# Kernel optimization log

Measured on AMD Instinct MI355X. Metric: run time of the kernel, lower is better.

The kernel has to match this reference:

```python
import math
import jax, jax.numpy as jnp
import numpy as np

B, S, D, H = 2, 2048, 2048, 16
HD = D // H  # head_dim = 128


def setup_inputs() -> dict:
    key = jax.random.key(0)
    ks = jax.random.split(key, 5)
    x = jax.random.normal(ks[0], (B, S, D), dtype=jnp.float32)
    # torch nn.Linear weights are [out_features, in_features]
    wq = jax.random.normal(ks[1], (D, D), dtype=jnp.float32) * 0.02
    wk = jax.random.normal(ks[2], (D, D), dtype=jnp.float32) * 0.02
    wv = jax.random.normal(ks[3], (D, D), dtype=jnp.float32) * 0.02
    wo = jax.random.normal(ks[4], (D, D), dtype=jnp.float32) * 0.02
    # llama-style rotary frequencies: freq_cis[t, i] = exp(1j * t / 10000^(2i/hd))
    inv_freq = 1.0 / (10000.0 ** (jnp.arange(0, HD, 2, dtype=jnp.float32) / HD))  # [HD/2]
    angles = jnp.arange(S, dtype=jnp.float32)[:, None] * inv_freq[None, :]  # [S, HD/2]
    freq_cos = jnp.cos(angles)
    freq_sin = jnp.sin(angles)
    # additive causal mask (0 on/below diagonal, large negative above)
    mask = jnp.triu(jnp.full((S, S), -1e9, dtype=jnp.float32), k=1)
    return {"x": x, "wq": wq, "wk": wk, "wv": wv, "wo": wo,
            "freq_cos": freq_cos, "freq_sin": freq_sin, "mask": mask}


def _rope(t, cos, sin):
    # t: [B, H, S, HD]; cos/sin: [S, HD/2]. Consecutive pairs form complex numbers.
    b, h, s, hd = t.shape
    tr = t.reshape(b, h, s, hd // 2, 2)
    re, im = tr[..., 0], tr[..., 1]
    c = cos[None, None, :, :]
    sn = sin[None, None, :, :]
    out_re = re * c - im * sn
    out_im = re * sn + im * c
    return jnp.stack([out_re, out_im], axis=-1).reshape(b, h, s, hd)


def reference(x, wq, wk, wv, wo, freq_cos, freq_sin, mask):
    b, s, d = x.shape
    hd = 2 * freq_cos.shape[-1]
    h = wq.shape[0] // hd
    # projections (torch Linear: y = x @ W.T)
    q = jnp.einsum('bsd,ed->bse', x, wq).reshape(b, s, h, hd).transpose(0, 2, 1, 3)
    k = jnp.einsum('bsd,ed->bse', x, wk).reshape(b, s, h, hd).transpose(0, 2, 1, 3)
    v = jnp.einsum('bsd,ed->bse', x, wv).reshape(b, s, h, hd).transpose(0, 2, 1, 3)
    q = _rope(q, freq_cos, freq_sin)
    k = _rope(k, freq_cos, freq_sin)
    scores = jnp.einsum('bhqd,bhkd->bhqk', q, k) / math.sqrt(hd)  # [B,H,S,S]
    scores = scores + mask[None, None, :, :]
    attn = jax.nn.softmax(scores, axis=-1)
    o = jnp.einsum('bhqk,bhkd->bhqd', attn, v)
    o = o.transpose(0, 2, 1, 3).reshape(b, s, h * hd)
    return jnp.einsum('bse,de->bsd', o, wo)
```

## Files before the change

kernel.cpp:

```cpp
#include <hip/hip_runtime.h>
#include <stdint.h>

#define BB  2
#define SS  2048
#define DD  2048
#define HH  16
#define HDD 128
#define MM  (BB * SS)

typedef __attribute__((ext_vector_type(8)))  short short8;
typedef __attribute__((ext_vector_type(4)))  float f32x4;
typedef __attribute__((ext_vector_type(16))) float f32x16;
typedef unsigned int   u32;
typedef unsigned short u16;
typedef __attribute__((ext_vector_type(4))) u16 u16x4;
typedef __attribute__((ext_vector_type(2))) u32 u32x2;
typedef __attribute__((ext_vector_type(4))) u32 u32x4;

static __device__ __forceinline__ u16 f2bf(float f) {
  u32 u = __builtin_bit_cast(u32, f);
  u32 r = u + 0x7fffu + ((u >> 16) & 1u);
  return (u16)(r >> 16);
}

static __device__ __forceinline__ u32 cvtpk(float a, float b) {
  u32 r;
  asm("v_cvt_pk_bf16_f32 %0, %1, %2" : "=v"(r) : "v"(a), "v"(b));
  return r;
}
static __device__ __forceinline__ void permswap(u32& a, u32& b) {
  asm volatile("v_permlane32_swap_b32 %0, %1" : "+v"(a), "+v"(b));
}

__global__ void cvt_all(const float* __restrict__ x,  const float* __restrict__ wq,
                        const float* __restrict__ wk, const float* __restrict__ wv,
                        const float* __restrict__ wo,
                        u16* __restrict__ xb, u16* __restrict__ wqkv,
                        u16* __restrict__ wob) {
  const int NX = (MM * DD) / 4;
  const int NW = (DD * DD) / 4;
  int i = blockIdx.x * blockDim.x + threadIdx.x;
  const float* s; u16* d; int off;
  if (i < NX) { s = x; d = xb; off = i; }
  else {
    int j = i - NX; int w = j >> 20; off = j & (NW - 1);
    s = (w == 0) ? wq : (w == 1) ? wk : (w == 2) ? wv : wo;
    d = (w < 3) ? (wqkv + (size_t)w * DD * DD) : wob;
  }
  f32x4 v = *(const f32x4*)(s + (size_t)off * 4);
  u16x4 o;
#pragma unroll
  for (int j = 0; j < 4; ++j) o[j] = f2bf(v[j]);
  *(u16x4*)(d + (size_t)off * 4) = o;
}

template <int MODE>
__global__ __launch_bounds__(256) void gemm2(const u16* __restrict__ A,
                                             const u16* __restrict__ Bw,
                                             u16* __restrict__ Cq,
                                             u16* __restrict__ Ck,
                                             u16* __restrict__ Cvt,
                                             float* __restrict__ Cf,
                                             int M, int N, int K,
                                             const float* __restrict__ fc,
                                             const float* __restrict__ fs) {
  __shared__ __align__(16) u16 Al[2][128 * 64];
  __shared__ __align__(16) u16 Bl[2][128 * 64];
  const int tid  = threadIdx.x;
  const int wave = tid >> 6, lane = tid & 63;
  const int m0 = blockIdx.y * 128, n0 = blockIdx.x * 128;
  const int wr = (wave >> 1) * 64, wc = (wave & 1) * 64;
  const int lrow = lane & 15, kh = lane >> 4;
  const int sk = lrow & 7;

  f32x4 acc[4][4] = {};

#define GSTAGE(T, BUF)                                                                  \
  {                                                                                     \
    int koff = (T) * 64;                                                                \
    _Pragma("unroll")                                                                   \
    for (int j_ = 0; j_ < 4; ++j_) {                                                    \
      int i_ = tid + j_ * 256;                                             \
      int r_ = i_ >> 3, c_ = i_ & 7;                                                    \
      int sc_ = (c_ ^ (r_ & 7)) * 8;                                                    \
      const u16* ga = A  + (size_t)(m0 + r_) * K + koff + sc_;                          \
      __builtin_amdgcn_global_load_lds((const __attribute__((address_space(1))) u32*)ga,\
                                       (__attribute__((address_space(3))) u32*)(&Al[BUF][0] + i_ * 8), \
                                       16, 0, 0);                                       \
      const u16* gb = Bw + (size_t)(n0 + r_) * K + koff + sc_;                          \
      __builtin_amdgcn_global_load_lds((const __attribute__((address_space(1))) u32*)gb,\
                                       (__attribute__((address_space(3))) u32*)(&Bl[BUF][0] + i_ * 8), \
                                       16, 0, 0);                                       \
    }                                                                                   \
  }

  const int NT = K / 64;
  GSTAGE(0, 0);
  for (int t = 0; t < NT; ++t) {
    const int bt = t & 1;
    if (t + 1 < NT) {
      GSTAGE(t + 1, bt ^ 1);
      asm volatile("s_waitcnt vmcnt(8)" ::: "memory");
    } else {
      asm volatile("s_waitcnt vmcnt(0)" ::: "memory");
    }
    __builtin_amdgcn_s_barrier();

    const u16* Ab = &Al[bt][0];
    const u16* Bb = &Bl[bt][0];
    short8 af[4][2], bf[4][2];
#pragma unroll
    for (int tt = 0; tt < 4; ++tt)
#pragma unroll
      for (int ks = 0; ks < 2; ++ks) {
        af[tt][ks] = *(const short8*)(Ab + (wr + tt * 16 + lrow) * 64 + ((ks * 4 + kh) ^ sk) * 8);
        bf[tt][ks] = *(const short8*)(Bb + (wc + tt * 16 + lrow) * 64 + ((ks * 4 + kh) ^ sk) * 8);
      }
#pragma unroll
    for (int mt = 0; mt < 4; ++mt)
#pragma unroll
      for (int nt = 0; nt < 4; ++nt)
#pragma unroll
        for (int ks = 0; ks < 2; ++ks)
          acc[mt][nt] = __builtin_amdgcn_mfma_f32_16x16x32_bf16(af[mt][ks], bf[nt][ks], acc[mt][nt], 0, 0, 0);

    __builtin_amdgcn_s_barrier();
  }
#undef GSTAGE

  const int dr = kh * 4;
  if constexpr (MODE == 1) {
#pragma unroll
    for (int mt = 0; mt < 4; ++mt)
#pragma unroll
      for (int nt = 0; nt < 4; ++nt)
#pragma unroll
        for (int i = 0; i < 4; ++i) {
          size_t r = (size_t)(m0 + wr + mt * 16 + dr + i);
          size_t c = (size_t)(n0 + wc + nt * 16 + lrow);
          Cf[r * N + c] = acc[mt][nt][i];
        }
  } else {
    const int region = n0 >> 11;
    if (region < 2) {
      u16* Cd = region ? Ck : Cq;
      const float sfac = region ? 1.f : 0.08838834764831845f * 1.44269504088896340736f;
#pragma unroll
      for (int mt = 0; mt < 4; ++mt)
#pragma unroll
        for (int nt = 0; nt < 4; ++nt) {
          int c  = n0 + wc + nt * 16 + lrow;
          int cl = c & 2047;
          int dh = cl & 127, pi = dh >> 1;
          float sgn = (dh & 1) ? 1.f : -1.f;
#pragma unroll
          for (int i = 0; i < 4; ++i) {
            int r  = m0 + wr + mt * 16 + dr + i;
            int s_ = r & (SS - 1);
            float cc_ = fc[s_ * 64 + pi] * sfac;
            float ss_ = fs[s_ * 64 + pi] * (sgn * sfac);
            float v  = acc[mt][nt][i];
            float pv = __shfl_xor(v, 1, 64);
            Cd[(size_t)r * 2048 + cl] = f2bf(v * cc_ + pv * ss_);
          }
        }
    } else {
#pragma unroll
      for (int mt = 0; mt < 4; ++mt)
#pragma unroll
        for (int nt = 0; nt < 4; ++nt) {
          int cl = (n0 - 4096) + wc + nt * 16 + lrow;
          int rr = m0 + wr + mt * 16 + dr;
          int b  = rr >> 11, s0 = rr & 2047;
          u16x4 pk;
#pragma unroll
          for (int i = 0; i < 4; ++i) pk[i] = f2bf(acc[mt][nt][i]);
          *(u16x4*)(Cvt + ((size_t)b * 2048 + cl) * 2048 + s0) = pk;
        }
    }
  }
}

__global__ __launch_bounds__(256, 2) void attn_kernel(const u16* __restrict__ Q,
                                                      const u16* __restrict__ K,
                                                      const u16* __restrict__ Vt,
                                                      u16* __restrict__ O) {
  __shared__ __align__(16) u16 Kl[2][64 * 128];
  __shared__ __align__(16) u16 Vl[2][128 * 64];

  const int tid = threadIdx.x, wave = tid >> 6, lane = tid & 63;
  const int l31 = lane & 31, hi = lane >> 5;
  const int bh = blockIdx.x, b = bh >> 4, h = bh & 15;
  const int y = blockIdx.y;
  const int qt = (y < 8) ? y : (23 - y);
  const size_t base    = ((size_t)b * SS) * DD + (size_t)h * HDD;
  const size_t vt_base = (size_t)bh * HDD * SS;
  const int swz = (l31 & 7) << 4;

#define STAGE(KT, BUF)                                                              \
  {                                                                                 \
    int k0s = (KT) * 64;                                                            \
    _Pragma("unroll")                                                               \
    for (int i_ = 0; i_ < 4; ++i_) {                                                \
      int idx = tid + i_ * 256;                                                     \
      int kr = idx >> 4, c_ = idx & 15;                                             \
      const u16* gk = K + base + (size_t)(k0s + kr) * DD + ((c_ ^ (kr & 7)) * 8);   \
      __builtin_amdgcn_global_load_lds((const __attribute__((address_space(1))) u32*)gk, \
                                       (__attribute__((address_space(3))) u32*)(&Kl[BUF][0] + idx * 8), \
                                       16, 0, 0);                                   \
      int dv = idx >> 3, c2 = idx & 7;                                              \
      const u16* gv = Vt + vt_base + (size_t)dv * SS + k0s + ((c2 ^ (dv & 7)) * 8); \
      __builtin_amdgcn_global_load_lds((const __attribute__((address_space(1))) u32*)gv, \
                                       (__attribute__((address_space(3))) u32*)(&Vl[BUF][0] + idx * 8), \
                                       16, 0, 0);                                   \
    }                                                                               \
  }

  const int qw = qt * 128 + wave * 32;
  const int q_ = qw + l31;

  short8 qf[8];
#pragma unroll
  for (int kc = 0; kc < 8; ++kc)
    qf[kc] = *(const short8*)(Q + base + (size_t)(qw + l31) * DD + kc * 16 + hi * 8);

  f32x16 oacc[4] = {};
  float m_i = -1e30f, l_p = 0.f;

  int buf = 0;
  STAGE(0, 0);

  const int ntiles = 2 * qt + 2;
  for (int kt = 0; kt < ntiles; ++kt) {
    const int k0 = kt * 64;
    if (kt + 1 < ntiles) {
      STAGE(kt + 1, buf ^ 1);
      asm volatile("s_waitcnt vmcnt(8)" ::: "memory");
    } else {
      asm volatile("s_waitcnt vmcnt(0)" ::: "memory");
    }
    __builtin_amdgcn_s_barrier();

    if (k0 <= qw + 31) {
      const u16* Kb_ = &Kl[buf][0];
      const u16* Vb_ = &Vl[buf][0];

      f32x16 st[2] = {};
      __builtin_amdgcn_s_setprio(1);
#pragma unroll
      for (int kc = 0; kc < 8; ++kc) {
        int by0 = (l31 * 256)        + ((kc * 32 + hi * 16) ^ swz);
        int by1 = ((32 + l31) * 256) + ((kc * 32 + hi * 16) ^ swz);
        short8 a0 = *(const short8*)(Kb_ + (by0 >> 1));
        short8 a1 = *(const short8*)(Kb_ + (by1 >> 1));
        st[0] = __builtin_amdgcn_mfma_f32_32x32x16_bf16(a0, qf[kc], st[0], 0, 0, 0);
        st[1] = __builtin_amdgcn_mfma_f32_32x32x16_bf16(a1, qf[kc], st[1], 0, 0, 0);
      }
      __builtin_amdgcn_s_setprio(0);

      float mx = -1e30f;
      if (k0 + 63 > qw) {
#pragma unroll
        for (int kb = 0; kb < 2; ++kb)
#pragma unroll
          for (int r = 0; r < 16; ++r) {
            float s = st[kb][r];
            int key = k0 + kb * 32 + (r & 3) + ((r >> 2) << 3) + (hi << 2);
            if (key > q_) s = -1e30f;
            st[kb][r] = s;
            mx = fmaxf(mx, s);
          }
      } else {
#pragma unroll
        for (int kb = 0; kb < 2; ++kb)
#pragma unroll
          for (int r = 0; r < 16; ++r) mx = fmaxf(mx, st[kb][r]);
      }
      mx = fmaxf(mx, __shfl_xor(mx, 32, 64));

      if (__any(mx > m_i + 8.f)) {
        float mn  = fmaxf(m_i, mx);
        float esc = exp2f(m_i - mn);
        m_i = mn; l_p *= esc;
#pragma unroll
        for (int db = 0; db < 4; ++db)
#pragma unroll
          for (int r = 0; r < 16; ++r) oacc[db][r] *= esc;
      }
      float sum = 0.f;
#pragma unroll
      for (int kb = 0; kb < 2; ++kb)
#pragma unroll
        for (int r = 0; r < 16; ++r) {
          float e = exp2f(st[kb][r] - m_i);
          st[kb][r] = e;
          sum += e;
        }
      l_p += sum;

      __builtin_amdgcn_s_setprio(1);
#pragma unroll
      for (int kb = 0; kb < 2; ++kb) {
#pragma unroll
        for (int half = 0; half < 2; ++half) {
          const int rb = half * 8;
          u32 w0 = cvtpk(st[kb][rb + 0], st[kb][rb + 1]);
          u32 w1 = cvtpk(st[kb][rb + 2], st[kb][rb + 3]);
          u32 w2 = cvtpk(st[kb][rb + 4], st[kb][rb + 5]);
          u32 w3 = cvtpk(st[kb][rb + 6], st[kb][rb + 7]);
          permswap(w0, w2);
          permswap(w1, w3);
          short8 pf = __builtin_bit_cast(short8, (u32x4){w0, w1, w2, w3});
          const int ktv = kb * 2 + half;
#pragma unroll
          for (int db = 0; db < 4; ++db) {
            int d = db * 32 + l31;
            int by = d * 128 + ((ktv * 32 + hi * 16) ^ swz);
            short8 vf = *(const short8*)(Vb_ + (by >> 1));
            oacc[db] = __builtin_amdgcn_mfma_f32_32x32x16_bf16(vf, pf, oacc[db], 0, 0, 0);
          }
        }
      }
      __builtin_amdgcn_s_setprio(0);
    }
    __builtin_amdgcn_s_barrier();
    buf ^= 1;
  }

  float lt  = l_p + __shfl_xor(l_p, 32, 64);
  float inv = 1.f / lt;
#pragma unroll
  for (int db = 0; db < 4; ++db)
#pragma unroll
    for (int g = 0; g < 4; ++g) {
      int d0 = db * 32 + 8 * g + 4 * hi;
      u32x2 pk;
      pk[0] = cvtpk(oacc[db][4 * g + 0] * inv, oacc[db][4 * g + 1] * inv);
      pk[1] = cvtpk(oacc[db][4 * g + 2] * inv, oacc[db][4 * g + 3] * inv);
      *(u32x2*)(O + base + (size_t)q_ * DD + d0) = pk;
    }
#undef STAGE
}

extern "C" void kernel_launch(void* const* d_in, const int* in_sizes, int n_in,
                              void* d_out, int out_size, void* d_ws, size_t ws_size,
                              hipStream_t stream) {
  (void)in_sizes; (void)n_in; (void)out_size; (void)ws_size;
  const float* x  = (const float*)d_in[0];
  const float* wq = (const float*)d_in[1];
  const float* wk = (const float*)d_in[2];
  const float* wv = (const float*)d_in[3];
  const float* wo = (const float*)d_in[4];
  const float* fc = (const float*)d_in[5];
  const float* fs = (const float*)d_in[6];
  float* out = (float*)d_out;

  const size_t XBUF = (size_t)MM * DD * 2;
  const size_t WBUF = (size_t)DD * DD * 2;
  char* ws = (char*)d_ws;
  u16* xb   = (u16*)(ws);
  u16* Qb   = (u16*)(ws + XBUF);
  u16* Kb   = (u16*)(ws + 2 * XBUF);
  u16* Vtb  = (u16*)(ws + 3 * XBUF);
  u16* wqkv = (u16*)(ws + 4 * XBUF);
  u16* wob  = (u16*)(ws + 4 * XBUF + 3 * WBUF);
  u16* Ob   = xb;

  const int ncv = (MM * DD) / 4 + 4 * ((DD * DD) / 4);
  cvt_all<<<ncv / 256, 256, 0, stream>>>(x, wq, wk, wv, wo, xb, wqkv, wob);

  gemm2<4><<<dim3(48, 32), 256, 0, stream>>>(xb, wqkv, Qb, Kb, Vtb, nullptr,
                                             MM, 3 * DD, DD, fc, fs);

  attn_kernel<<<dim3(32, 16), 256, 0, stream>>>(Qb, Kb, Vtb, Ob);

  gemm2<1><<<dim3(16, 32), 256, 0, stream>>>(Ob, wob, nullptr, nullptr, nullptr, out,
                                             MM, DD, DD, nullptr, nullptr);
}
```

Baseline: 247.8 us.

## Use 256x256 8-wave tile with phased quarter-tile loads for QKV GEMM

Replaces the 128x128 four-wave QKV projection GEMM with a 256x256 tile run by eight waves (512 threads, one block per CU). Each K-step is split into four phases that issue the global-to-LDS loads for the next tiles in halves, interleaved with MFMA bursts under raised priority and explicit vmcnt waits. The aim is more operand reuse per LDS byte and better overlap of memory traffic with matrix math. The cost is 128KB of LDS, a large accumulator register footprint, and only 384 blocks, which may leave some CUs idle in the final wave.

Result: slower. 266.7 us (+7.6%).

```diff
diff --git a/kernel.cpp b/kernel.cpp
--- a/kernel.cpp
+++ b/kernel.cpp
@@ -54,16 +54,156 @@
   *(u16x4*)(d + (size_t)off * 4) = o;
 }
 
-template <int MODE>
-__global__ __launch_bounds__(256) void gemm2(const u16* __restrict__ A,
-                                             const u16* __restrict__ Bw,
-                                             u16* __restrict__ Cq,
-                                             u16* __restrict__ Ck,
-                                             u16* __restrict__ Cvt,
-                                             float* __restrict__ Cf,
-                                             int M, int N, int K,
-                                             const float* __restrict__ fc,
-                                             const float* __restrict__ fs) {
+__global__ __launch_bounds__(512, 1) void gemm8_qkv(const u16* __restrict__ A,
+                                                    const u16* __restrict__ Bw,
+                                                    u16* __restrict__ Cq,
+                                                    u16* __restrict__ Ck,
+                                                    u16* __restrict__ Cvt,
+                                                    const float* __restrict__ fc,
+                                                    const float* __restrict__ fs) {
+  const int K = DD;
+  __shared__ __align__(16) u16 Al[2][256 * 64];
+  __shared__ __align__(16) u16 Bl[2][256 * 64];
+  const int tid = threadIdx.x, lane = tid & 63;
+  const int wid = tid >> 6;
+  const int wm = wid >> 2, wn = wid & 3;
+  const int m0b = blockIdx.y * 256, n0b = blockIdx.x * 256;
+  const int lrow = lane & 15, kh = lane >> 4;
+  const int sk = lrow & 7;
+
+  f32x4 acc[8][4] = {};
+
+#define STGH(Tt, HT) do {                                                             \
+    int k0s = (Tt) * 64; int bs = (Tt) & 1;                                           \
+    u16* dst = (((HT) >= 2) ? &Bl[bs][0] : &Al[bs][0]) + ((HT) & 1) * 8192;           \
+    const u16* srcb = ((HT) >= 2) ? Bw : A;                                           \
+    int rb = (((HT) >= 2) ? n0b : m0b) + ((HT) & 1) * 128;                            \
+    _Pragma("unroll")                                                                 \
+    for (int j_ = 0; j_ < 2; ++j_) {                                                  \
+      int i_ = tid + j_ * 512;                                                        \
+      int r_ = i_ >> 3, c_ = i_ & 7;                                                  \
+      const u16* g_ = srcb + (size_t)(rb + r_) * K + k0s + ((c_ ^ (r_ & 7)) * 8);     \
+      __builtin_amdgcn_global_load_lds((const __attribute__((address_space(1))) u32*)g_, \
+          (__attribute__((address_space(3))) u32*)(dst + i_ * 8), 16, 0, 0);          \
+    } } while (0)
+
+#define RDA(MH)                                                                       \
+    _Pragma("unroll")                                                                 \
+    for (int f = 0; f < 4; ++f)                                                       \
+      _Pragma("unroll")                                                               \
+      for (int ks = 0; ks < 2; ++ks)                                                  \
+        a[f][ks] = *(const short8*)(Ab + ((MH) * 128 + wm * 64 + f * 16 + lrow) * 64  \
+                                       + (((ks * 4 + kh) ^ sk) * 8));
+
+#define RDB(NH)                                                                       \
+    _Pragma("unroll")                                                                 \
+    for (int g = 0; g < 2; ++g)                                                       \
+      _Pragma("unroll")                                                               \
+      for (int ks = 0; ks < 2; ++ks)                                                  \
+        b[g][ks] = *(const short8*)(Bb + ((NH) * 128 + wn * 32 + g * 16 + lrow) * 64  \
+                                       + (((ks * 4 + kh) ^ sk) * 8));
+
+#define PHASE_SYNC()                                                                  \
+    __builtin_amdgcn_s_barrier();                                                     \
+    asm volatile("s_waitcnt lgkmcnt(0)" ::: "memory");                                \
+    __builtin_amdgcn_sched_barrier(0);
+
+#define MFMA16(MH, NH)                                                                \
+    __builtin_amdgcn_s_setprio(1);                                                    \
+    _Pragma("unroll")                                                                 \
+    for (int f = 0; f < 4; ++f)                                                       \
+      _Pragma("unroll")                                                               \
+      for (int g = 0; g < 2; ++g)                                                     \
+        _Pragma("unroll")                                                             \
+        for (int ks = 0; ks < 2; ++ks)                                                \
+          acc[(MH) * 4 + f][(NH) * 2 + g] = __builtin_amdgcn_mfma_f32_16x16x32_bf16(  \
+              a[f][ks], b[g][ks], acc[(MH) * 4 + f][(NH) * 2 + g], 0, 0, 0);          \
+    __builtin_amdgcn_s_setprio(0);
+
+  STGH(0, 0); STGH(0, 2); STGH(0, 1); STGH(0, 3);
+  STGH(1, 0); STGH(1, 3); STGH(1, 1);
+  asm volatile("s_waitcnt vmcnt(6)" ::: "memory");
+  __builtin_amdgcn_s_barrier();
+
+  const int NT = K / 64;
+  for (int t = 0; t < NT; ++t) {
+    const int pb = t & 1;
+    const u16* Ab = &Al[pb][0];
+    const u16* Bb = &Bl[pb][0];
+    short8 a[4][2], b[2][2];
+
+    RDA(0); RDB(0);
+    if (t + 1 < NT) STGH(t + 1, 2);
+    PHASE_SYNC(); MFMA16(0, 0);
+    __builtin_amdgcn_s_barrier();
+
+    RDB(1);
+    if (t + 2 < NT) STGH(t + 2, 0);
+    PHASE_SYNC(); MFMA16(0, 1);
+    __builtin_amdgcn_s_barrier();
+
+    RDA(1);
+    if (t + 2 < NT) STGH(t + 2, 3);
+    PHASE_SYNC(); MFMA16(1, 1);
+    __builtin_amdgcn_s_barrier();
+
+    RDB(0);
+    if (t + 2 < NT) STGH(t + 2, 1);
+    if (t <= NT - 4) { asm volatile("s_waitcnt vmcnt(6)" ::: "memory"); }
+    else             { asm volatile("s_waitcnt vmcnt(0)" ::: "memory"); }
+    PHASE_SYNC(); MFMA16(1, 0);
+    __builtin_amdgcn_s_barrier();
+  }
+#undef STGH
+#undef RDA
+#undef RDB
+#undef PHASE_SYNC
+#undef MFMA16
+
+  const int dr = kh * 4;
+  const int region = n0b >> 11;
+  if (region < 2) {
+    u16* Cd = region ? Ck : Cq;
+    const float sfac = region ? 1.f : 0.08838834764831845f * 1.44269504088896340736f;
+#pragma unroll
+    for (int mf = 0; mf < 8; ++mf)
+#pragma unroll
+      for (int nf = 0; nf < 4; ++nf) {
+        int c  = n0b + (nf >> 1) * 128 + wn * 32 + (nf & 1) * 16 + lrow;
+        int cl = c & 2047;
+        int dh = cl & 127, pi = dh >> 1;
+        float sgn = (dh & 1) ? 1.f : -1.f;
+#pragma unroll
+        for (int i = 0; i < 4; ++i) {
+          int r  = m0b + (mf >> 2) * 128 + wm * 64 + (mf & 3) * 16 + dr + i;
+          int s_ = r & (SS - 1);
+          float cc_ = fc[s_ * 64 + pi] * sfac;
+          float ss_ = fs[s_ * 64 + pi] * (sgn * sfac);
+          float v  = acc[mf][nf][i];
+          float pv = __shfl_xor(v, 1, 64);
+          Cd[(size_t)r * 2048 + cl] = f2bf(v * cc_ + pv * ss_);
+        }
+      }
+  } else {
+#pragma unroll
+    for (int mf = 0; mf < 8; ++mf)
+#pragma unroll
+      for (int nf = 0; nf < 4; ++nf) {
+        int cl = (n0b - 4096) + (nf >> 1) * 128 + wn * 32 + (nf & 1) * 16 + lrow;
+        int rr = m0b + (mf >> 2) * 128 + wm * 64 + (mf & 3) * 16 + dr;
+        int b_ = rr >> 11, s0 = rr & 2047;
+        u16x4 pk;
+#pragma unroll
+        for (int i = 0; i < 4; ++i) pk[i] = f2bf(acc[mf][nf][i]);
+        *(u16x4*)(Cvt + ((size_t)b_ * 2048 + cl) * 2048 + s0) = pk;
+      }
+  }
+}
+
+__global__ __launch_bounds__(256) void gemm_o(const u16* __restrict__ A,
+                                              const u16* __restrict__ Bw,
+                                              float* __restrict__ Cf,
+                                              int M, int N, int K) {
   __shared__ __align__(16) u16 Al[2][128 * 64];
   __shared__ __align__(16) u16 Bl[2][128 * 64];
   const int tid  = threadIdx.x;
@@ -80,7 +220,7 @@
     int koff = (T) * 64;                                                                \
     _Pragma("unroll")                                                                   \
     for (int j_ = 0; j_ < 4; ++j_) {                                                    \
-      int i_ = tid + j_ * 256;                                             \
+      int i_ = tid + j_ * 256;                                                          \
       int r_ = i_ >> 3, c_ = i_ & 7;                                                    \
       int sc_ = (c_ ^ (r_ & 7)) * 8;                                                    \
       const u16* ga = A  + (size_t)(m0 + r_) * K + koff + sc_;                          \
@@ -129,56 +269,16 @@
 #undef GSTAGE
 
   const int dr = kh * 4;
-  if constexpr (MODE == 1) {
-#pragma unroll
-    for (int mt = 0; mt < 4; ++mt)
-#pragma unroll
-      for (int nt = 0; nt < 4; ++nt)
-#pragma unroll
-        for (int i = 0; i < 4; ++i) {
-          size_t r = (size_t)(m0 + wr + mt * 16 + dr + i);
-          size_t c = (size_t)(n0 + wc + nt * 16 + lrow);
-          Cf[r * N + c] = acc[mt][nt][i];
-        }
-  } else {
-    const int region = n0 >> 11;
-    if (region < 2) {
-      u16* Cd = region ? Ck : Cq;
-      const float sfac = region ? 1.f : 0.08838834764831845f * 1.44269504088896340736f;
-#pragma unroll
-      for (int mt = 0; mt < 4; ++mt)
-#pragma unroll
-        for (int nt = 0; nt < 4; ++nt) {
-          int c  = n0 + wc + nt * 16 + lrow;
-          int cl = c & 2047;
-          int dh = cl & 127, pi = dh >> 1;
-          float sgn = (dh & 1) ? 1.f : -1.f;
-#pragma unroll
-          for (int i = 0; i < 4; ++i) {
-            int r  = m0 + wr + mt * 16 + dr + i;
-            int s_ = r & (SS - 1);
-            float cc_ = fc[s_ * 64 + pi] * sfac;
-            float ss_ = fs[s_ * 64 + pi] * (sgn * sfac);
-            float v  = acc[mt][nt][i];
-            float pv = __shfl_xor(v, 1, 64);
-            Cd[(size_t)r * 2048 + cl] = f2bf(v * cc_ + pv * ss_);
-          }
-        }
-    } else {
-#pragma unroll
-      for (int mt = 0; mt < 4; ++mt)
-#pragma unroll
-        for (int nt = 0; nt < 4; ++nt) {
-          int cl = (n0 - 4096) + wc + nt * 16 + lrow;
-          int rr = m0 + wr + mt * 16 + dr;
-          int b  = rr >> 11, s0 = rr & 2047;
-          u16x4 pk;
-#pragma unroll
-          for (int i = 0; i < 4; ++i) pk[i] = f2bf(acc[mt][nt][i]);
-          *(u16x4*)(Cvt + ((size_t)b * 2048 + cl) * 2048 + s0) = pk;
-        }
-    }
-  }
+#pragma unroll
+  for (int mt = 0; mt < 4; ++mt)
+#pragma unroll
+    for (int nt = 0; nt < 4; ++nt)
+#pragma unroll
+      for (int i = 0; i < 4; ++i) {
+        size_t r = (size_t)(m0 + wr + mt * 16 + dr + i);
+        size_t c = (size_t)(n0 + wc + nt * 16 + lrow);
+        Cf[r * N + c] = acc[mt][nt][i];
+      }
 }
 
 __global__ __launch_bounds__(256, 2) void attn_kernel(const u16* __restrict__ Q,
@@ -369,11 +469,9 @@
   const int ncv = (MM * DD) / 4 + 4 * ((DD * DD) / 4);
   cvt_all<<<ncv / 256, 256, 0, stream>>>(x, wq, wk, wv, wo, xb, wqkv, wob);
 
-  gemm2<4><<<dim3(48, 32), 256, 0, stream>>>(xb, wqkv, Qb, Kb, Vtb, nullptr,
-                                             MM, 3 * DD, DD, fc, fs);
+  gemm8_qkv<<<dim3(24, 16), 512, 0, stream>>>(xb, wqkv, Qb, Kb, Vtb, fc, fs);
 
   attn_kernel<<<dim3(32, 16), 256, 0, stream>>>(Qb, Kb, Vtb, Ob);
 
-  gemm2<1><<<dim3(16, 32), 256, 0, stream>>>(Ob, wob, nullptr, nullptr, nullptr, out,
-                                             MM, DD, DD, nullptr, nullptr);
-}
+  gemm_o<<<dim3(16, 32), 256, 0, stream>>>(Ob, wob, out, MM, DD, DD);
+}
```

## Single-buffer GEMM LDS for occupancy, add XCD block swizzle, grid-stride convert

Applied to the files above, without the earlier changes.

The GEMM drops LDS double buffering for a single buffer with two __syncthreads per k-step and sets launch_bounds(256,5), aiming for more resident blocks per CU. Block indices are remapped with an 8-way swizzle over a 1D grid, so neighbouring tiles that share data land on the same XCD and reuse its L2. The fp32-to-bf16 conversion kernel becomes a grid-stride loop over a fixed 2048-block grid. The risk is that global loads no longer overlap with MFMA compute inside a block, so latency hiding depends on occupancy alone.

Result: slower. 682.4 us (+175.3%).

```diff
diff --git a/kernel.cpp b/kernel.cpp
--- a/kernel.cpp
+++ b/kernel.cpp
@@ -39,43 +39,50 @@
                         u16* __restrict__ wob) {
   const int NX = (MM * DD) / 4;
   const int NW = (DD * DD) / 4;
-  int i = blockIdx.x * blockDim.x + threadIdx.x;
-  const float* s; u16* d; int off;
-  if (i < NX) { s = x; d = xb; off = i; }
-  else {
-    int j = i - NX; int w = j >> 20; off = j & (NW - 1);
-    s = (w == 0) ? wq : (w == 1) ? wk : (w == 2) ? wv : wo;
-    d = (w < 3) ? (wqkv + (size_t)w * DD * DD) : wob;
-  }
-  f32x4 v = *(const f32x4*)(s + (size_t)off * 4);
-  u16x4 o;
-#pragma unroll
-  for (int j = 0; j < 4; ++j) o[j] = f2bf(v[j]);
-  *(u16x4*)(d + (size_t)off * 4) = o;
+  const int total = NX + 4 * NW;
+  for (int i = blockIdx.x * blockDim.x + threadIdx.x; i < total;
+       i += gridDim.x * blockDim.x) {
+    const float* s; u16* d; int off;
+    if (i < NX) { s = x; d = xb; off = i; }
+    else {
+      int j = i - NX; int w = j >> 20; off = j & (NW - 1);
+      s = (w == 0) ? wq : (w == 1) ? wk : (w == 2) ? wv : wo;
+      d = (w < 3) ? (wqkv + (size_t)w * DD * DD) : wob;
+    }
+    f32x4 v = *(const f32x4*)(s + (size_t)off * 4);
+    u16x4 o;
+#pragma unroll
+    for (int j = 0; j < 4; ++j) o[j] = f2bf(v[j]);
+    *(u16x4*)(d + (size_t)off * 4) = o;
+  }
 }
 
 template <int MODE>
-__global__ __launch_bounds__(256) void gemm2(const u16* __restrict__ A,
-                                             const u16* __restrict__ Bw,
-                                             u16* __restrict__ Cq,
-                                             u16* __restrict__ Ck,
-                                             u16* __restrict__ Cvt,
-                                             float* __restrict__ Cf,
-                                             int M, int N, int K,
-                                             const float* __restrict__ fc,
-                                             const float* __restrict__ fs) {
-  __shared__ __align__(16) u16 Al[2][128 * 64];
-  __shared__ __align__(16) u16 Bl[2][128 * 64];
+__global__ __launch_bounds__(256, 5) void gemm2(const u16* __restrict__ A,
+                                                const u16* __restrict__ Bw,
+                                                u16* __restrict__ Cq,
+                                                u16* __restrict__ Ck,
+                                                u16* __restrict__ Cvt,
+                                                float* __restrict__ Cf,
+                                                int M, int N, int K, int nbx,
+                                                const float* __restrict__ fc,
+                                                const float* __restrict__ fs) {
+  __shared__ __align__(16) u16 Al[128 * 64];
+  __shared__ __align__(16) u16 Bl[128 * 64];
   const int tid  = threadIdx.x;
   const int wave = tid >> 6, lane = tid & 63;
-  const int m0 = blockIdx.y * 128, n0 = blockIdx.x * 128;
+  const int cpx = gridDim.x >> 3;
+  const int bid = blockIdx.x;
+  const int swzb = (bid & 7) * cpx + (bid >> 3);
+  const int bx = swzb % nbx, by = swzb / nbx;
+  const int m0 = by * 128, n0 = bx * 128;
   const int wr = (wave >> 1) * 64, wc = (wave & 1) * 64;
   const int lrow = lane & 15, kh = lane >> 4;
   const int sk = lrow & 7;
 
   f32x4 acc[4][4] = {};
 
-#define GSTAGE(T, BUF)                                                                  \
+#define GSTAGE(T)                                                                       \
   {                                                                                     \
     int koff = (T) * 64;                                                                \
     _Pragma("unroll")                                                                   \
@@ -85,36 +92,28 @@
       int sc_ = (c_ ^ (r_ & 7)) * 8;                                                    \
       const u16* ga = A  + (size_t)(m0 + r_) * K + koff + sc_;                          \
       __builtin_amdgcn_global_load_lds((const __attribute__((address_space(1))) u32*)ga,\
-                                       (__attribute__((address_space(3))) u32*)(&Al[BUF][0] + i_ * 8), \
+                                       (__attribute__((address_space(3))) u32*)(Al + i_ * 8), \
                                        16, 0, 0);                                       \
       const u16* gb = Bw + (size_t)(n0 + r_) * K + koff + sc_;                          \
       __builtin_amdgcn_global_load_lds((const __attribute__((address_space(1))) u32*)gb,\
-                                       (__attribute__((address_space(3))) u32*)(&Bl[BUF][0] + i_ * 8), \
+                                       (__attribute__((address_space(3))) u32*)(Bl + i_ * 8), \
                                        16, 0, 0);                                       \
     }                                                                                   \
   }
 
   const int NT = K / 64;
-  GSTAGE(0, 0);
   for (int t = 0; t < NT; ++t) {
-    const int bt = t & 1;
-    if (t + 1 < NT) {
-      GSTAGE(t + 1, bt ^ 1);
-      asm volatile("s_waitcnt vmcnt(8)" ::: "memory");
-    } else {
-      asm volatile("s_waitcnt vmcnt(0)" ::: "memory");
-    }
-    __builtin_amdgcn_s_barrier();
-
-    const u16* Ab = &Al[bt][0];
-    const u16* Bb = &Bl[bt][0];
+    if (t) __syncthreads();
+    GSTAGE(t);
+    __syncthreads();
+
     short8 af[4][2], bf[4][2];
 #pragma unroll
     for (int tt = 0; tt < 4; ++tt)
 #pragma unroll
       for (int ks = 0; ks < 2; ++ks) {
-        af[tt][ks] = *(const short8*)(Ab + (wr + tt * 16 + lrow) * 64 + ((ks * 4 + kh) ^ sk) * 8);
-        bf[tt][ks] = *(const short8*)(Bb + (wc + tt * 16 + lrow) * 64 + ((ks * 4 + kh) ^ sk) * 8);
+        af[tt][ks] = *(const short8*)(Al + (wr + tt * 16 + lrow) * 64 + ((ks * 4 + kh) ^ sk) * 8);
+        bf[tt][ks] = *(const short8*)(Bl + (wc + tt * 16 + lrow) * 64 + ((ks * 4 + kh) ^ sk) * 8);
       }
 #pragma unroll
     for (int mt = 0; mt < 4; ++mt)
@@ -123,8 +122,6 @@
 #pragma unroll
         for (int ks = 0; ks < 2; ++ks)
           acc[mt][nt] = __builtin_amdgcn_mfma_f32_16x16x32_bf16(af[mt][ks], bf[nt][ks], acc[mt][nt], 0, 0, 0);
-
-    __builtin_amdgcn_s_barrier();
   }
 #undef GSTAGE
 
@@ -366,14 +363,13 @@
   u16* wob  = (u16*)(ws + 4 * XBUF + 3 * WBUF);
   u16* Ob   = xb;
 
-  const int ncv = (MM * DD) / 4 + 4 * ((DD * DD) / 4);
-  cvt_all<<<ncv / 256, 256, 0, stream>>>(x, wq, wk, wv, wo, xb, wqkv, wob);
-
-  gemm2<4><<<dim3(48, 32), 256, 0, stream>>>(xb, wqkv, Qb, Kb, Vtb, nullptr,
-                                             MM, 3 * DD, DD, fc, fs);
+  cvt_all<<<2048, 256, 0, stream>>>(x, wq, wk, wv, wo, xb, wqkv, wob);
+
+  gemm2<4><<<1536, 256, 0, stream>>>(xb, wqkv, Qb, Kb, Vtb, nullptr,
+                                     MM, 3 * DD, DD, 48, fc, fs);
 
   attn_kernel<<<dim3(32, 16), 256, 0, stream>>>(Qb, Kb, Vtb, Ob);
 
-  gemm2<1><<<dim3(16, 32), 256, 0, stream>>>(Ob, wob, nullptr, nullptr, nullptr, out,
-                                             MM, DD, DD, nullptr, nullptr);
-}
+  gemm2<1><<<512, 256, 0, stream>>>(Ob, wob, nullptr, nullptr, nullptr, out,
+                                    MM, DD, DD, 16, nullptr, nullptr);
+}
```
